# Kernel tuning notes

Measured on AMD Instinct MI355X. Metric: run time of the kernel, lower is better.

## Reference

```python
import jax, jax.numpy as jnp
import numpy as np

D_MODEL = 1024


def setup_inputs() -> dict:
    key = jax.random.key(0)
    ks = jax.random.split(key, 11)
    B, Sq, Skv, D = 16, 2048, 2048, D_MODEL
    s = 1.0 / np.sqrt(D)
    return {
        "q": jax.random.normal(ks[0], (B, Sq, D), jnp.float32),
        "k": jax.random.normal(ks[1], (B, Skv, D), jnp.float32),
        "v": jax.random.normal(ks[2], (B, Skv, D), jnp.float32),
        "Wq": jax.random.normal(ks[3], (D, D), jnp.float32) * s,
        "bq": jnp.zeros((D,), jnp.float32),
        "Wk": jax.random.normal(ks[4], (D, D), jnp.float32) * s,
        "bk": jnp.zeros((D,), jnp.float32),
        "Wv": jax.random.normal(ks[5], (D, D), jnp.float32) * s,
        "bv": jnp.zeros((D,), jnp.float32),
        "Wo": jax.random.normal(ks[6], (D, D), jnp.float32) * s,
        "bo": jnp.zeros((D,), jnp.float32),
    }


def reference(q, k, v, Wq, bq, Wk, bk, Wv, bv, Wo, bo):
    D = q.shape[-1]
    # Projections (torch Linear: x @ W^T + b; here W stored as [in, out])
    query = q @ Wq + bq          # [B, Sq, D]
    key_p = k @ Wk + bk          # [B, Skv, D]
    value = v @ Wv + bv          # [B, Skv, D]
    # Scaled dot-product attention, scale by sqrt(d_model) (single head)
    scores = jnp.einsum('bqd,bkd->bqk', query / jnp.sqrt(jnp.float32(D)), key_p)
    attn = jax.nn.softmax(scores, axis=-1)   # dropout p=0.0 -> identity
    out = jnp.einsum('bqk,bkd->bqd', attn, value)
    return out @ Wo + bo
```

## Files before the change

kernel.cpp:

```cpp
#include <hip/hip_runtime.h>

typedef unsigned int u32;
typedef unsigned short u16;
typedef __attribute__((ext_vector_type(8))) __bf16 bf16x8;
typedef __attribute__((ext_vector_type(4))) float f32x4;

typedef __attribute__((address_space(1))) void as1_void;
typedef __attribute__((address_space(3))) void as3_void;

__device__ __forceinline__ u16 f2bf(float f){
  u32 u = __builtin_bit_cast(u32, f);
  return (u16)((u + 0x7FFFu + ((u >> 16) & 1u)) >> 16);
}
__device__ __forceinline__ float bf2f(u16 h){
  u32 u = ((u32)h) << 16;
  return __builtin_bit_cast(float, u);
}

__device__ __forceinline__ void gload16(const void* g, void* l){
  __builtin_amdgcn_global_load_lds((as1_void*)(unsigned long long)g, (as3_void*)l, 16, 0, 0);
}
__device__ __forceinline__ bf16x8 ldfrag(const char* p){
  return __builtin_bit_cast(bf16x8, *(const uint4*)p);
}

__global__ void wcast(const float* __restrict__ W, float scale, u16* __restrict__ out){
  __shared__ float t[32][33];
  int bx = blockIdx.x * 32, by = blockIdx.y * 32;
  int tx = threadIdx.x, ty = threadIdx.y;
  #pragma unroll
  for (int i = 0; i < 32; i += 8) t[ty + i][tx] = W[(size_t)(bx + ty + i) * 1024 + by + tx];
  __syncthreads();
  #pragma unroll
  for (int i = 0; i < 32; i += 8)
    out[(size_t)(by + ty + i) * 1024 + bx + tx] = f2bf(scale * t[tx][ty + i]);
}

__global__ __launch_bounds__(256) void castbf(const float* __restrict__ in, u16* __restrict__ out, int n8){
  int stride = gridDim.x * blockDim.x;
  for (int i = blockIdx.x * blockDim.x + threadIdx.x; i < n8; i += stride){
    const float4* p = (const float4*)(in + (size_t)i * 8);
    float4 f0 = p[0], f1 = p[1];
    union { uint4 u; u16 h[8]; } uu;
    uu.h[0]=f2bf(f0.x); uu.h[1]=f2bf(f0.y); uu.h[2]=f2bf(f0.z); uu.h[3]=f2bf(f0.w);
    uu.h[4]=f2bf(f1.x); uu.h[5]=f2bf(f1.y); uu.h[6]=f2bf(f1.z); uu.h[7]=f2bf(f1.w);
    ((uint4*)out)[i] = uu.u;
  }
}

__global__ __launch_bounds__(256) void softmax_rows(u16* __restrict__ S){
  __shared__ float red[8];
  size_t row = blockIdx.x;
  uint4* p = (uint4*)(S + row * 2048);
  int tid = threadIdx.x;
  int lane = tid & 63, wave = tid >> 6;
  union { uint4 u4; u16 h[8]; } uu;
  uu.u4 = p[tid];
  float v[8];
  float m = -1e30f;
  #pragma unroll
  for (int j = 0; j < 8; j++){ v[j] = bf2f(uu.h[j]); m = fmaxf(m, v[j]); }
  #pragma unroll
  for (int o = 32; o; o >>= 1) m = fmaxf(m, __shfl_xor(m, o));
  if (lane == 0) red[wave] = m;
  __syncthreads();
  m = fmaxf(fmaxf(red[0], red[1]), fmaxf(red[2], red[3]));
  float s = 0.f;
  #pragma unroll
  for (int j = 0; j < 8; j++){ v[j] = __expf(v[j] - m); s += v[j]; }
  #pragma unroll
  for (int o = 32; o; o >>= 1) s += __shfl_xor(s, o);
  if (lane == 0) red[4 + wave] = s;
  __syncthreads();
  s = red[4] + red[5] + red[6] + red[7];
  float inv = 1.f / s;
  #pragma unroll
  for (int j = 0; j < 8; j++) uu.h[j] = f2bf(v[j] * inv);
  p[tid] = uu.u4;
}


template<int MO, int N0>
__device__ __forceinline__ void pm(f32x4 (&acc)[8][4], bf16x8 (&a)[4][2], bf16x8 (&b)[2][2]){
  __builtin_amdgcn_s_setprio(1);
  #pragma unroll
  for (int ks = 0; ks < 2; ks++)
    #pragma unroll
    for (int mm = 0; mm < 4; mm++)
      #pragma unroll
      for (int nn = 0; nn < 2; nn++)
        acc[MO + mm][N0 + nn] = __builtin_amdgcn_mfma_f32_16x16x32_bf16(
            a[mm][ks], b[nn][ks], acc[MO + mm][N0 + nn], 0, 0, 0);
  __builtin_amdgcn_s_setprio(0);
}

template<int BIAS, int OUTF32>
__global__ __launch_bounds__(512, 2) void gemm8(
    const u16* __restrict__ A, const u16* __restrict__ B, void* __restrict__ C,
    const float* __restrict__ bias, float bscale, int NT,
    long long sA, long long sB, long long sC,
    int lda, int ldb, int ldc, int gx, int gxy, int TPB)
{
  __shared__ u16 sm[2][2][16384];
  char* smb = (char*)sm;

  int tid = threadIdx.x;
  int lane = tid & 63, wave = tid >> 6;
  int wr = wave >> 2, wc = wave & 3;
  int l15 = lane & 15, l4 = lane >> 4;

  int b = blockIdx.x;
  int lin0 = ((b & 7) * 32 + (b >> 3)) * TPB;

  int r = tid >> 3, cl = tid & 7;
  int ldsb = r * 128 + cl * 16;
  u32 aoff[4], boff[4];
  #pragma unroll
  for (int i = 0; i < 4; i++){
    int row = i * 64 + r;
    int ksw = (cl ^ (r & 7)) * 8;
    aoff[i] = (u32)(((u32)row * (u32)lda + (u32)ksw) * 2u);
    boff[i] = (u32)(((u32)row * (u32)ldb + (u32)ksw) * 2u);
  }
  u32 ardo[2], brdo[2];
  #pragma unroll
  for (int ks = 0; ks < 2; ks++){
    u32 sw = (u32)(((ks * 4 + l4) ^ (l15 & 7)) * 16);
    ardo[ks] = (u32)(wr * 16384 + l15 * 128) + sw;
    brdo[ks] = (u32)(wc * 8192 + l15 * 128) + sw;
  }

  auto tcoord = [&](int lin, int& x, int& y, int& z){
    z = lin / gxy; int rem = lin - z * gxy; y = rem / gx; x = rem - y * gx;
  };
  auto abase = [&](int lin){ int x, y, z; tcoord(lin, x, y, z);
    return (const char*)(A + (long long)z * sA + (size_t)(x * 256) * lda); };
  auto bbase = [&](int lin){ int x, y, z; tcoord(lin, x, y, z);
    return (const char*)(B + (long long)z * sB + (size_t)(y * 256) * ldb); };

  int tx, ty, tz;
  tcoord(lin0, tx, ty, tz);
  int row0 = tx * 256, col0 = ty * 256;
  long long zbC = tz;

  float bc0[4], bc1[4];
  if (BIAS){
    int xx, yy, zz;
    tcoord(lin0, xx, yy, zz);
    int c0 = yy * 256 + wc * 64 + l15;
    #pragma unroll
    for (int n = 0; n < 4; n++) bc0[n] = bscale * bias[c0 + n * 16];
    tcoord(lin0 + (TPB > 1 ? 1 : 0), xx, yy, zz);
    c0 = yy * 256 + wc * 64 + l15;
    #pragma unroll
    for (int n = 0; n < 4; n++) bc1[n] = bscale * bias[c0 + n * 16];
  }

  const char* AgM = abase(lin0);
  const char* AgP = AgM;
  const char* BgP = bbase(lin0);
  int km = 1, kp = 2, jm = 0, jp = 0, kk = 0, jj = 0;

#define STA(bse, i, kq, bb) gload16((bse) + aoff[i] + (size_t)(kq) * 128, smb + (bb) * 65536 + (i) * 8192 + ldsb)
#define STB(bse, i, kq, bb) gload16((bse) + boff[i] + (size_t)(kq) * 128, smb + (bb) * 65536 + 32768 + (i) * 8192 + ldsb)

  STA(AgM, 0, 0, 0); STA(AgM, 2, 0, 0);
  STB(BgP, 0, 0, 0); STB(BgP, 1, 0, 0); STB(BgP, 2, 0, 0); STB(BgP, 3, 0, 0);
  STA(AgM, 1, 0, 0); STA(AgM, 3, 0, 0);
  STA(AgM, 0, 1, 1); STA(AgM, 2, 1, 1);
  STB(BgP, 0, 1, 1); STB(BgP, 1, 1, 1); STB(BgP, 2, 1, 1); STB(BgP, 3, 1, 1);
  asm volatile("s_waitcnt vmcnt(6)" ::: "memory");
  __builtin_amdgcn_s_barrier();

  f32x4 acc[8][4] = {};
  bf16x8 aLo[4][2], aHi[4][2], b01[2][2], b23[2][2];
  int S = TPB * NT;

  #pragma unroll
  for (int mm = 0; mm < 4; mm++)
    #pragma unroll
    for (int ks = 0; ks < 2; ks++)
      aLo[mm][ks] = ldfrag(smb + mm * 2048 + ardo[ks]);

  for (int s = 0; s < S; s++){
    int cur = s & 1;
    const char* Ab = smb + cur * 65536;
    const char* Bb = Ab + 32768;
    const char* AbN = smb + (cur ^ 1) * 65536;
    bool st1 = (s + 1 < S), st2 = (s + 2 < S);

    if (st1){ STA(AgM, 1, km, cur ^ 1); STA(AgM, 3, km, cur ^ 1); }
    #pragma unroll
    for (int nn = 0; nn < 2; nn++)
      #pragma unroll
      for (int ks = 0; ks < 2; ks++)
        b01[nn][ks] = ldfrag(Bb + nn * 2048 + brdo[ks]);
    #pragma unroll
    for (int nn = 0; nn < 2; nn++)
      #pragma unroll
      for (int ks = 0; ks < 2; ks++)
        b23[nn][ks] = ldfrag(Bb + (2 + nn) * 2048 + brdo[ks]);
    __builtin_amdgcn_s_barrier();
    pm<0, 0>(acc, aLo, b01);
    __builtin_amdgcn_s_barrier();

    if (st2){ STA(AgP, 0, kp, cur); STA(AgP, 2, kp, cur); }
    #pragma unroll
    for (int mm = 0; mm < 4; mm++)
      #pragma unroll
      for (int ks = 0; ks < 2; ks++)
        aHi[mm][ks] = ldfrag(Ab + (4 + mm) * 2048 + ardo[ks]);
    __builtin_amdgcn_s_barrier();
    pm<0, 2>(acc, aLo, b23);
    __builtin_amdgcn_s_barrier();

    if (st2){ STB(BgP, 0, kp, cur); STB(BgP, 1, kp, cur); }
    __builtin_amdgcn_s_barrier();
    pm<4, 2>(acc, aHi, b23);
    __builtin_amdgcn_s_barrier();

    if (st2){ STB(BgP, 2, kp, cur); STB(BgP, 3, kp, cur); }
    if (s < S - 2) asm volatile("s_waitcnt vmcnt(6)" ::: "memory");
    else           asm volatile("s_waitcnt vmcnt(0)" ::: "memory");
    __builtin_amdgcn_s_barrier();
    if (st1){
      #pragma unroll
      for (int mm = 0; mm < 4; mm++)
        #pragma unroll
        for (int ks = 0; ks < 2; ks++)
          aLo[mm][ks] = ldfrag(AbN + mm * 2048 + ardo[ks]);
    }
    pm<4, 0>(acc, aHi, b01);
    __builtin_amdgcn_s_barrier();

    if (++km == NT){ km = 0; if (++jm < TPB) AgM = abase(lin0 + jm); }
    if (++kp == NT){ kp = 0; if (++jp < TPB){ AgP = abase(lin0 + jp); BgP = bbase(lin0 + jp); } }
    if (++kk == NT){
      kk = 0;
      #pragma unroll
      for (int m = 0; m < 8; m++){
        #pragma unroll
        for (int n = 0; n < 4; n++){
          int gr0 = row0 + wr * 128 + m * 16 + l4 * 4;
          int gc  = col0 + wc * 64 + n * 16 + l15;
          float bcol = BIAS ? (jj == 0 ? bc0[n] : bc1[n]) : 0.f;
          #pragma unroll
          for (int j = 0; j < 4; j++){
            float vv = acc[m][n][j] + bcol;
            int gr = gr0 + j;
            if (OUTF32) ((float*)C)[zbC * sC + (size_t)gr * ldc + gc] = vv;
            else        ((u16*) C)[zbC * sC + (size_t)gr * ldc + gc] = f2bf(vv);
          }
          acc[m][n] = (f32x4){0.f, 0.f, 0.f, 0.f};
        }
      }
      if (++jj < TPB){
        tcoord(lin0 + jj, tx, ty, tz);
        row0 = tx * 256; col0 = ty * 256; zbC = tz;
      }
    }
  }
#undef STA
#undef STB
}

extern "C" void kernel_launch(void* const* d_in, const int* in_sizes, int n_in,
                              void* d_out, int out_size, void* d_ws, size_t ws_size,
                              hipStream_t stream){
  const float* q  = (const float*)d_in[0];
  const float* k  = (const float*)d_in[1];
  const float* v  = (const float*)d_in[2];
  const float* Wq = (const float*)d_in[3];
  const float* bq = (const float*)d_in[4];
  const float* Wk = (const float*)d_in[5];
  const float* bk = (const float*)d_in[6];
  const float* Wv = (const float*)d_in[7];
  const float* bv = (const float*)d_in[8];
  const float* Wo = (const float*)d_in[9];
  const float* bo = (const float*)d_in[10];

  char* ws = (char*)d_ws;
  const size_t MB = (size_t)1 << 20;
  u16* Wqt = (u16*)(ws + 0 * MB);
  u16* Wkt = (u16*)(ws + 2 * MB);
  u16* Wvt = (u16*)(ws + 4 * MB);
  u16* Wot = (u16*)(ws + 6 * MB);
  u16* Qp  = (u16*)(ws + 8 * MB);
  u16* Kp  = (u16*)(ws + 72 * MB);
  u16* Vt  = (u16*)(ws + 136 * MB);
  u16* S   = (u16*)(ws + 200 * MB);
  u16* O   = (u16*)(ws + 328 * MB);
  u16* X   = (u16*)(ws + 200 * MB);
  float* out = (float*)d_out;

  dim3 wb(32, 8);
  wcast<<<dim3(32, 32), wb, 0, stream>>>(Wq, 1.f / 32.f, Wqt);
  wcast<<<dim3(32, 32), wb, 0, stream>>>(Wk, 1.f, Wkt);
  wcast<<<dim3(32, 32), wb, 0, stream>>>(Wv, 1.f, Wvt);
  wcast<<<dim3(32, 32), wb, 0, stream>>>(Wo, 1.f, Wot);

  const int n8 = 16 * 2048 * 1024 / 8;

  castbf<<<dim3(2048), 256, 0, stream>>>(q, X, n8);
  gemm8<1,0><<<dim3(256), 512, 0, stream>>>(X, Wqt, Qp, bq, 1.f/32.f,
      16, 0, 0, 0, 1024, 1024, 1024, 128, 512, 2);
  castbf<<<dim3(2048), 256, 0, stream>>>(k, X, n8);
  gemm8<1,0><<<dim3(256), 512, 0, stream>>>(X, Wkt, Kp, bk, 1.f,
      16, 0, 0, 0, 1024, 1024, 1024, 128, 512, 2);
  castbf<<<dim3(2048), 256, 0, stream>>>(v, X, n8);
  gemm8<0,0><<<dim3(256), 512, 0, stream>>>(Wvt, X, Vt, nullptr, 0.f,
      16, 0, 2048LL * 1024, 1024LL * 2048, 1024, 1024, 2048, 4, 32, 2);
  gemm8<0,0><<<dim3(256), 512, 0, stream>>>(Qp, Kp, S, nullptr, 0.f,
      16, 2048LL * 1024, 2048LL * 1024, 2048LL * 2048, 1024, 1024, 2048, 8, 64, 4);
  softmax_rows<<<dim3(32768), 256, 0, stream>>>(S);
  gemm8<1,0><<<dim3(256), 512, 0, stream>>>(S, Vt, O, bv, 1.f,
      32, 2048LL * 2048, 1024LL * 2048, 2048LL * 1024, 2048, 2048, 1024, 8, 32, 2);
  gemm8<1,1><<<dim3(256), 512, 0, stream>>>(O, Wot, out, bo, 1.f,
      16, 0, 0, 0, 1024, 1024, 1024, 128, 512, 2);
}
```

Measured before the change: 740.6 us.

## Fuse fp32-to-bf16 input casts into projection GEMM tile loads

Removes the three standalone castbf passes over q, k and v. The projection GEMMs now read fp32 tiles straight from global memory into registers, convert them to bf16 and write them into swizzled LDS, instead of using the bf16 global_load_lds path. This saves a full write and re-read of the bf16 intermediate for each input. In exchange, the fp32 operand goes through a register-staged load with different waitcnt bookkeeping, and the A fragments are no longer hoisted ahead of the loop, which may reduce latency hiding in the main loop.

```diff
diff --git a/kernel.cpp b/kernel.cpp
--- a/kernel.cpp
+++ b/kernel.cpp
@@ -23,6 +23,12 @@
 __device__ __forceinline__ bf16x8 ldfrag(const char* p){
   return __builtin_bit_cast(bf16x8, *(const uint4*)p);
 }
+__device__ __forceinline__ uint4 cvt8(float4 a, float4 b){
+  union { uint4 u; __bf16 h[8]; } uu;
+  uu.h[0]=(__bf16)a.x; uu.h[1]=(__bf16)a.y; uu.h[2]=(__bf16)a.z; uu.h[3]=(__bf16)a.w;
+  uu.h[4]=(__bf16)b.x; uu.h[5]=(__bf16)b.y; uu.h[6]=(__bf16)b.z; uu.h[7]=(__bf16)b.w;
+  return uu.u;
+}
 
 __global__ void wcast(const float* __restrict__ W, float scale, u16* __restrict__ out){
   __shared__ float t[32][33];
@@ -34,18 +40,6 @@
   #pragma unroll
   for (int i = 0; i < 32; i += 8)
     out[(size_t)(by + ty + i) * 1024 + bx + tx] = f2bf(scale * t[tx][ty + i]);
-}
-
-__global__ __launch_bounds__(256) void castbf(const float* __restrict__ in, u16* __restrict__ out, int n8){
-  int stride = gridDim.x * blockDim.x;
-  for (int i = blockIdx.x * blockDim.x + threadIdx.x; i < n8; i += stride){
-    const float4* p = (const float4*)(in + (size_t)i * 8);
-    float4 f0 = p[0], f1 = p[1];
-    union { uint4 u; u16 h[8]; } uu;
-    uu.h[0]=f2bf(f0.x); uu.h[1]=f2bf(f0.y); uu.h[2]=f2bf(f0.z); uu.h[3]=f2bf(f0.w);
-    uu.h[4]=f2bf(f1.x); uu.h[5]=f2bf(f1.y); uu.h[6]=f2bf(f1.z); uu.h[7]=f2bf(f1.w);
-    ((uint4*)out)[i] = uu.u;
-  }
 }
 
 __global__ __launch_bounds__(256) void softmax_rows(u16* __restrict__ S){
@@ -94,13 +88,14 @@
   __builtin_amdgcn_s_setprio(0);
 }
 
-template<int BIAS, int OUTF32>
+template<int AF32, int BF32, int BIAS, int OUTF32>
 __global__ __launch_bounds__(512, 2) void gemm8(
-    const u16* __restrict__ A, const u16* __restrict__ B, void* __restrict__ C,
+    const void* __restrict__ A, const void* __restrict__ B, void* __restrict__ C,
     const float* __restrict__ bias, float bscale, int NT,
     long long sA, long long sB, long long sC,
     int lda, int ldb, int ldc, int gx, int gxy, int TPB)
 {
+  constexpr bool HOIST = (!AF32 && !BF32);
   __shared__ u16 sm[2][2][16384];
   char* smb = (char*)sm;
 
@@ -114,13 +109,15 @@
 
   int r = tid >> 3, cl = tid & 7;
   int ldsb = r * 128 + cl * 16;
+  int ldsw = r * 128 + ((cl ^ (r & 7)) * 16);
   u32 aoff[4], boff[4];
   #pragma unroll
   for (int i = 0; i < 4; i++){
     int row = i * 64 + r;
-    int ksw = (cl ^ (r & 7)) * 8;
-    aoff[i] = (u32)(((u32)row * (u32)lda + (u32)ksw) * 2u);
-    boff[i] = (u32)(((u32)row * (u32)ldb + (u32)ksw) * 2u);
+    if constexpr (AF32) aoff[i] = (u32)(((u32)row * (u32)lda + (u32)(cl * 8)) * 4u);
+    else                aoff[i] = (u32)(((u32)row * (u32)lda + (u32)((cl ^ (r & 7)) * 8)) * 2u);
+    if constexpr (BF32) boff[i] = (u32)(((u32)row * (u32)ldb + (u32)(cl * 8)) * 4u);
+    else                boff[i] = (u32)(((u32)row * (u32)ldb + (u32)((cl ^ (r & 7)) * 8)) * 2u);
   }
   u32 ardo[2], brdo[2];
   #pragma unroll
@@ -134,9 +131,9 @@
     z = lin / gxy; int rem = lin - z * gxy; y = rem / gx; x = rem - y * gx;
   };
   auto abase = [&](int lin){ int x, y, z; tcoord(lin, x, y, z);
-    return (const char*)(A + (long long)z * sA + (size_t)(x * 256) * lda); };
+    return (const char*)A + ((long long)z * sA + (long long)(x * 256) * lda) * (AF32 ? 4 : 2); };
   auto bbase = [&](int lin){ int x, y, z; tcoord(lin, x, y, z);
-    return (const char*)(B + (long long)z * sB + (size_t)(y * 256) * ldb); };
+    return (const char*)B + ((long long)z * sB + (long long)(y * 256) * ldb) * (BF32 ? 4 : 2); };
 
   int tx, ty, tz;
   tcoord(lin0, tx, ty, tz);
@@ -164,23 +161,66 @@
 #define STA(bse, i, kq, bb) gload16((bse) + aoff[i] + (size_t)(kq) * 128, smb + (bb) * 65536 + (i) * 8192 + ldsb)
 #define STB(bse, i, kq, bb) gload16((bse) + boff[i] + (size_t)(kq) * 128, smb + (bb) * 65536 + 32768 + (i) * 8192 + ldsb)
 
-  STA(AgM, 0, 0, 0); STA(AgM, 2, 0, 0);
-  STB(BgP, 0, 0, 0); STB(BgP, 1, 0, 0); STB(BgP, 2, 0, 0); STB(BgP, 3, 0, 0);
-  STA(AgM, 1, 0, 0); STA(AgM, 3, 0, 0);
-  STA(AgM, 0, 1, 1); STA(AgM, 2, 1, 1);
-  STB(BgP, 0, 1, 1); STB(BgP, 1, 1, 1); STB(BgP, 2, 1, 1); STB(BgP, 3, 1, 1);
-  asm volatile("s_waitcnt vmcnt(6)" ::: "memory");
+  if constexpr (HOIST){
+    STA(AgM, 0, 0, 0); STA(AgM, 2, 0, 0);
+    STB(BgP, 0, 0, 0); STB(BgP, 1, 0, 0); STB(BgP, 2, 0, 0); STB(BgP, 3, 0, 0);
+    STA(AgM, 1, 0, 0); STA(AgM, 3, 0, 0);
+    STA(AgM, 0, 1, 1); STA(AgM, 2, 1, 1);
+    STB(BgP, 0, 1, 1); STB(BgP, 1, 1, 1); STB(BgP, 2, 1, 1); STB(BgP, 3, 1, 1);
+    asm volatile("s_waitcnt vmcnt(6)" ::: "memory");
+  } else {
+    if constexpr (!AF32){
+      STA(AgM, 0, 0, 0); STA(AgM, 2, 0, 0); STA(AgM, 1, 0, 0); STA(AgM, 3, 0, 0);
+      STA(AgM, 0, 1, 1); STA(AgM, 2, 1, 1);
+    }
+    if constexpr (!BF32){
+      STB(BgP, 0, 0, 0); STB(BgP, 1, 0, 0); STB(BgP, 2, 0, 0); STB(BgP, 3, 0, 0);
+      STB(BgP, 0, 1, 1); STB(BgP, 1, 1, 1); STB(BgP, 2, 1, 1); STB(BgP, 3, 1, 1);
+    }
+    if constexpr (AF32){
+      #pragma unroll
+      for (int t = 0; t < 2; t++){
+        float4 x0[4], x1[4];
+        #pragma unroll
+        for (int i = 0; i < 4; i++){
+          const float4* p = (const float4*)(AgP + aoff[i] + (u32)t * 256u);
+          x0[i] = p[0]; x1[i] = p[1];
+        }
+        #pragma unroll
+        for (int i = 0; i < 4; i++)
+          *(uint4*)(smb + t * 65536 + i * 8192 + ldsw) = cvt8(x0[i], x1[i]);
+      }
+    }
+    if constexpr (BF32){
+      #pragma unroll
+      for (int t = 0; t < 2; t++){
+        float4 x0[4], x1[4];
+        #pragma unroll
+        for (int i = 0; i < 4; i++){
+          const float4* p = (const float4*)(BgP + boff[i] + (u32)t * 256u);
+          x0[i] = p[0]; x1[i] = p[1];
+        }
+        #pragma unroll
+        for (int i = 0; i < 4; i++)
+          *(uint4*)(smb + t * 65536 + 32768 + i * 8192 + ldsw) = cvt8(x0[i], x1[i]);
+      }
+    }
+    asm volatile("s_waitcnt vmcnt(0) lgkmcnt(0)" ::: "memory");
+  }
   __builtin_amdgcn_s_barrier();
 
   f32x4 acc[8][4] = {};
   bf16x8 aLo[4][2], aHi[4][2], b01[2][2], b23[2][2];
+  float4 av0[4], av1[4], bv0[4], bv1[4];
   int S = TPB * NT;
 
-  #pragma unroll
-  for (int mm = 0; mm < 4; mm++)
-    #pragma unroll
-    for (int ks = 0; ks < 2; ks++)
-      aLo[mm][ks] = ldfrag(smb + mm * 2048 + ardo[ks]);
+  if constexpr (HOIST){
+    #pragma unroll
+    for (int mm = 0; mm < 4; mm++)
+      #pragma unroll
+      for (int ks = 0; ks < 2; ks++)
+        aLo[mm][ks] = ldfrag(smb + mm * 2048 + ardo[ks]);
+  }
 
   for (int s = 0; s < S; s++){
     int cur = s & 1;
@@ -189,7 +229,33 @@
     const char* AbN = smb + (cur ^ 1) * 65536;
     bool st1 = (s + 1 < S), st2 = (s + 2 < S);
 
-    if (st1){ STA(AgM, 1, km, cur ^ 1); STA(AgM, 3, km, cur ^ 1); }
+    if constexpr (AF32){
+      if (st2){
+        #pragma unroll
+        for (int i = 0; i < 4; i++){
+          const float4* p = (const float4*)(AgP + aoff[i] + (u32)kp * 256u);
+          av0[i] = p[0]; av1[i] = p[1];
+        }
+      }
+    } else {
+      if (st1){ STA(AgM, 1, km, cur ^ 1); STA(AgM, 3, km, cur ^ 1); }
+    }
+    if constexpr (BF32){
+      if (st2){
+        #pragma unroll
+        for (int i = 0; i < 4; i++){
+          const float4* p = (const float4*)(BgP + boff[i] + (u32)kp * 256u);
+          bv0[i] = p[0]; bv1[i] = p[1];
+        }
+      }
+    }
+    if constexpr (!HOIST){
+      #pragma unroll
+      for (int mm = 0; mm < 4; mm++)
+        #pragma unroll
+        for (int ks = 0; ks < 2; ks++)
+          aLo[mm][ks] = ldfrag(Ab + mm * 2048 + ardo[ks]);
+    }
     #pragma unroll
     for (int nn = 0; nn < 2; nn++)
       #pragma unroll
@@ -204,36 +270,78 @@
     pm<0, 0>(acc, aLo, b01);
     __builtin_amdgcn_s_barrier();
 
-    if (st2){ STA(AgP, 0, kp, cur); STA(AgP, 2, kp, cur); }
-    #pragma unroll
-    for (int mm = 0; mm < 4; mm++)
-      #pragma unroll
-      for (int ks = 0; ks < 2; ks++)
-        aHi[mm][ks] = ldfrag(Ab + (4 + mm) * 2048 + ardo[ks]);
+    if constexpr (!AF32){
+      if (st2){ STA(AgP, 0, kp, cur); STA(AgP, 2, kp, cur); }
+    }
+    if constexpr (HOIST){
+      #pragma unroll
+      for (int mm = 0; mm < 4; mm++)
+        #pragma unroll
+        for (int ks = 0; ks < 2; ks++)
+          aHi[mm][ks] = ldfrag(Ab + (4 + mm) * 2048 + ardo[ks]);
+    }
     __builtin_amdgcn_s_barrier();
     pm<0, 2>(acc, aLo, b23);
     __builtin_amdgcn_s_barrier();
 
-    if (st2){ STB(BgP, 0, kp, cur); STB(BgP, 1, kp, cur); }
+    if constexpr (BF32){
+      if (st2){
+        char* W = smb + cur * 65536 + 32768;
+        #pragma unroll
+        for (int i = 0; i < 4; i++)
+          *(uint4*)(W + i * 8192 + ldsw) = cvt8(bv0[i], bv1[i]);
+      }
+    } else {
+      if (st2){ STB(BgP, 0, kp, cur); STB(BgP, 1, kp, cur); }
+    }
+    if constexpr (!HOIST){
+      #pragma unroll
+      for (int mm = 0; mm < 4; mm++)
+        #pragma unroll
+        for (int ks = 0; ks < 2; ks++)
+          aHi[mm][ks] = ldfrag(Ab + (4 + mm) * 2048 + ardo[ks]);
+    }
     __builtin_amdgcn_s_barrier();
     pm<4, 2>(acc, aHi, b23);
     __builtin_amdgcn_s_barrier();
 
-    if (st2){ STB(BgP, 2, kp, cur); STB(BgP, 3, kp, cur); }
-    if (s < S - 2) asm volatile("s_waitcnt vmcnt(6)" ::: "memory");
-    else           asm volatile("s_waitcnt vmcnt(0)" ::: "memory");
-    __builtin_amdgcn_s_barrier();
-    if (st1){
-      #pragma unroll
-      for (int mm = 0; mm < 4; mm++)
-        #pragma unroll
-        for (int ks = 0; ks < 2; ks++)
-          aLo[mm][ks] = ldfrag(AbN + mm * 2048 + ardo[ks]);
+    if constexpr (!BF32){
+      if (st2){ STB(BgP, 2, kp, cur); STB(BgP, 3, kp, cur); }
+    }
+    if constexpr (AF32){
+      if (st2){
+        char* W = smb + cur * 65536;
+        #pragma unroll
+        for (int i = 0; i < 4; i++)
+          *(uint4*)(W + i * 8192 + ldsw) = cvt8(av0[i], av1[i]);
+      }
+    }
+    {
+      constexpr int VN = AF32 ? 4 : (BF32 ? 2 : 6);
+      if (s < S - 2){
+        if constexpr (VN == 4) asm volatile("s_waitcnt vmcnt(4)" ::: "memory");
+        else if constexpr (VN == 2) asm volatile("s_waitcnt vmcnt(2)" ::: "memory");
+        else asm volatile("s_waitcnt vmcnt(6)" ::: "memory");
+      } else {
+        asm volatile("s_waitcnt vmcnt(0)" ::: "memory");
+      }
+    }
+    __builtin_amdgcn_s_barrier();
+    if constexpr (HOIST){
+      if (st1){
+        #pragma unroll
+        for (int mm = 0; mm < 4; mm++)
+          #pragma unroll
+          for (int ks = 0; ks < 2; ks++)
+            aLo[mm][ks] = ldfrag(AbN + mm * 2048 + ardo[ks]);
+      }
     }
     pm<4, 0>(acc, aHi, b01);
     __builtin_amdgcn_s_barrier();
 
-    if (++km == NT){ km = 0; if (++jm < TPB) AgM = abase(lin0 + jm); }
+    if constexpr (!AF32){
+      if (++km == NT){ km = 0; if (++jm < TPB) AgM = abase(lin0 + jm); }
+    }
     if (++kp == NT){ kp = 0; if (++jp < TPB){ AgP = abase(lin0 + jp); BgP = bbase(lin0 + jp); } }
     if (++kk == NT){
       kk = 0;
@@ -290,7 +398,6 @@
   u16* Vt  = (u16*)(ws + 136 * MB);
   u16* S   = (u16*)(ws + 200 * MB);
   u16* O   = (u16*)(ws + 328 * MB);
-  u16* X   = (u16*)(ws + 200 * MB);
   float* out = (float*)d_out;
 
   dim3 wb(32, 8);
@@ -299,22 +406,17 @@
   wcast<<<dim3(32, 32), wb, 0, stream>>>(Wv, 1.f, Wvt);
   wcast<<<dim3(32, 32), wb, 0, stream>>>(Wo, 1.f, Wot);
 
-  const int n8 = 16 * 2048 * 1024 / 8;
-
-  castbf<<<dim3(2048), 256, 0, stream>>>(q, X, n8);
-  gemm8<1,0><<<dim3(256), 512, 0, stream>>>(X, Wqt, Qp, bq, 1.f/32.f,
+  gemm8<1,0,1,0><<<dim3(256), 512, 0, stream>>>(q, Wqt, Qp, bq, 1.f/32.f,
       16, 0, 0, 0, 1024, 1024, 1024, 128, 512, 2);
-  castbf<<<dim3(2048), 256, 0, stream>>>(k, X, n8);
-  gemm8<1,0><<<dim3(256), 512, 0, stream>>>(X, Wkt, Kp, bk, 1.f,
+  gemm8<1,0,1,0><<<dim3(256), 512, 0, stream>>>(k, Wkt, Kp, bk, 1.f,
       16, 0, 0, 0, 1024, 1024, 1024, 128, 512, 2);
-  castbf<<<dim3(2048), 256, 0, stream>>>(v, X, n8);
-  gemm8<0,0><<<dim3(256), 512, 0, stream>>>(Wvt, X, Vt, nullptr, 0.f,
+  gemm8<0,1,0,0><<<dim3(256), 512, 0, stream>>>(Wvt, v, Vt, nullptr, 0.f,
       16, 0, 2048LL * 1024, 1024LL * 2048, 1024, 1024, 2048, 4, 32, 2);
-  gemm8<0,0><<<dim3(256), 512, 0, stream>>>(Qp, Kp, S, nullptr, 0.f,
+  gemm8<0,0,0,0><<<dim3(256), 512, 0, stream>>>(Qp, Kp, S, nullptr, 0.f,
       16, 2048LL * 1024, 2048LL * 1024, 2048LL * 2048, 1024, 1024, 2048, 8, 64, 4);
   softmax_rows<<<dim3(32768), 256, 0, stream>>>(S);
-  gemm8<1,0><<<dim3(256), 512, 0, stream>>>(S, Vt, O, bv, 1.f,
+  gemm8<0,0,1,0><<<dim3(256), 512, 0, stream>>>(S, Vt, O, bv, 1.f,
       32, 2048LL * 2048, 1024LL * 2048, 2048LL * 1024, 2048, 2048, 1024, 8, 32, 2);
-  gemm8<1,1><<<dim3(256), 512, 0, stream>>>(O, Wot, out, bo, 1.f,
+  gemm8<0,0,1,1><<<dim3(256), 512, 0, stream>>>(O, Wot, out, bo, 1.f,
       16, 0, 0, 0, 1024, 1024, 1024, 128, 512, 2);
 }
```

Measured after the change: 1.091 ms. 47.3% more time.
